# Kernel optimization log

Hardware: AMD Instinct MI355X
Metric: run time of the kernel (lower is better)

Reference implementation:

```python
import jax, jax.numpy as jnp
import numpy as np

N = 50000
F_IN = 256
F_OUT = 256
K = 5
E = 1_600_000
SQRT_2PI = float(np.sqrt(2.0 * np.pi))
SQRT_2 = float(np.sqrt(2.0))


def _ex_relu(mu, sigma):
    # expected value of relu(Normal(mu, sigma)) with sigma = variance
    is_zero = sigma == 0
    safe_sigma = jnp.where(is_zero, 1e-10, sigma)
    sqrt_sigma = jnp.sqrt(safe_sigma)
    w = mu / sqrt_sigma
    nr = sqrt_sigma * (jnp.exp(-0.5 * w * w) / SQRT_2PI
                       + 0.5 * w * (1.0 + jax.lax.erf(w / SQRT_2)))
    return jnp.where(is_zero, jnp.maximum(mu, 0.0), nr)


def _conv(h, src, dst):
    # SimpleConv(aggr='add', combine_root='self_loop'):
    # out[d] = h[d] + sum_{(s,d) in edges} h[s];  h: [K, N, O]
    agg = jnp.zeros_like(h).at[:, dst, :].add(h[:, src, :])
    return h + agg


def setup_inputs() -> dict:
    key = jax.random.key(0)
    ks = jax.random.split(key, 7)
    x = jax.random.normal(ks[0], (N, F_IN), dtype=jnp.float32)
    edges = jax.random.randint(ks[1], (2, E), 0, N, dtype=jnp.int64)
    mask = jax.random.randint(ks[2], (N, F_IN), 0, 2) == 1  # True = missing
    logp = jax.random.normal(ks[3], (K,), dtype=jnp.float32)
    means = jax.random.normal(ks[4], (K, F_IN), dtype=jnp.float32)
    logvars = jax.random.normal(ks[5], (K, F_IN), dtype=jnp.float32)
    weight = jax.random.normal(ks[6], (F_IN, F_OUT), dtype=jnp.float32) * (1.414 / np.sqrt(F_IN + F_OUT) * np.sqrt(6.0))
    bias = jnp.zeros((F_OUT,), dtype=jnp.float32)
    return {"x": x, "edges": edges, "mask": mask, "logp": logp,
            "means": means, "logvars": logvars, "weight": weight, "bias": bias}


def reference(x, edges, mask, logp, means, logvars, weight, bias):
    src, dst = edges[0], edges[1]
    variances = jnp.exp(logvars)                                   # [K, F]
    m = mask[None, :, :]                                           # [1, N, F]
    mean_mat = jnp.where(m, means[:, None, :], x[None, :, :])      # [K, N, F]
    var_mat = jnp.where(m, variances[:, None, :], 0.0)             # [K, N, F]

    transform_x = jnp.einsum('knf,fo->kno', mean_mat, weight) + bias
    transform_covs = jnp.einsum('knf,fo->kno', var_mat, weight * weight)

    conv_x = _conv(transform_x, src, dst)                          # [K, N, O]
    conv_covs = _conv(transform_covs, src, dst)                    # [K, N, O]

    expected_x = _ex_relu(conv_x, conv_covs)                       # [K, N, O]

    # GMM responsibilities over components
    diff2 = (mean_mat - means[:, None, :]) ** 2 / variances[:, None, :]
    log_n = (-0.5 * jnp.sum(diff2, axis=2)
             - 0.5 * F_IN * np.log(2.0 * np.pi)
             - 0.5 * jnp.sum(logvars))                             # [K, N]
    gamma = jax.nn.softmax(logp[:, None] + log_n, axis=0)          # [K, N]

    return jnp.sum(expected_x * gamma[:, :, None], axis=0)         # [N, O]
```

## Files before the change

kernel.cpp:

```cpp
#include <hip/hip_runtime.h>
#include <math.h>

#define F 256
#define KMIX 5
#define RECB 640
#define GR 16
#define GS 3136

typedef __attribute__((ext_vector_type(8))) short bf16x8;
typedef __attribute__((ext_vector_type(4))) float f32x4;

__device__ __forceinline__ float bf2f(unsigned short u) {
  union { unsigned int i; float f; } v; v.i = ((unsigned int)u) << 16; return v.f;
}
__device__ __forceinline__ unsigned short f2bf(float f) {
  union { float f; unsigned int i; } v; v.f = f;
  unsigned int u = v.i;
  unsigned int r = (u + 0x7fffu + ((u >> 16) & 1u)) >> 16;
  return (unsigned short)r;
}

__device__ __forceinline__ f32x4 MFMA(bf16x8 a, bf16x8 b, f32x4 c) {
  return __builtin_amdgcn_mfma_f32_16x16x32_bf16(a, b, c, 0, 0, 0);
}

__device__ __forceinline__ float ex_relu_fast(float mu, float sig) {
  const float c1 = 1.2732395447f;
  const float c2 = 2.5464790895f;
  float t = mu * mu;
  float u = t + c1 * sig;
  float v = t + c2 * sig + 1e-20f;
  float r = __builtin_amdgcn_rsqf(v);
  return 0.5f * mu + 0.5f * u * r;
}

__global__ void kzero(unsigned int* p, long long n) {
  long long i = (long long)blockIdx.x * blockDim.x + threadIdx.x;
  long long stride = (long long)gridDim.x * blockDim.x;
  for (; i < n; i += stride) p[i] = 0u;
}

__global__ __launch_bounds__(256) void k_tab(const float* __restrict__ logvars,
                                             float* __restrict__ ivar) {
  int i = blockIdx.x * 256 + threadIdx.x;
  if (i < KMIX * F) ivar[i] = __expf(-logvars[i]);
}

__global__ __launch_bounds__(256) void k_prep(
    const float* __restrict__ x, const int* __restrict__ mask,
    const float* __restrict__ logp, const float* __restrict__ means,
    const float* __restrict__ ivar,
    unsigned char* __restrict__ rec, float* __restrict__ gamma, int Npad, int N) {
  int wave = threadIdx.x >> 6, lane = threadIdx.x & 63;
  int n = blockIdx.x * 4 + wave;
  if (n >= N) return;
  int f0 = lane * 4;
  const float4 xv4 = *(const float4*)(x + (size_t)n * F + f0);
  const int4 mv4 = *(const int4*)(mask + (size_t)n * F + f0);
  float xv[4] = {xv4.x, xv4.y, xv4.z, xv4.w};
  int mv[4] = {mv4.x, mv4.y, mv4.z, mv4.w};
  unsigned char* rn = rec + (size_t)n * RECB;
  ushort4 xm;
  xm.x = mv[0] ? (unsigned short)0 : f2bf(xv[0]);
  xm.y = mv[1] ? (unsigned short)0 : f2bf(xv[1]);
  xm.z = mv[2] ? (unsigned short)0 : f2bf(xv[2]);
  xm.w = mv[3] ? (unsigned short)0 : f2bf(xv[3]);
  *(ushort4*)(rn + lane * 8) = xm;
  unsigned int nib = (mv[0] ? 1u : 0u) | (mv[1] ? 2u : 0u) |
                     (mv[2] ? 4u : 0u) | (mv[3] ? 8u : 0u);
  unsigned int wbits = nib << ((lane & 7) * 4);
  wbits |= __shfl_xor(wbits, 1, 64);
  wbits |= __shfl_xor(wbits, 2, 64);
  wbits |= __shfl_xor(wbits, 4, 64);
  if ((lane & 7) == 0) *(unsigned int*)(rn + 512 + ((lane >> 3) << 2)) = wbits;
  float lg[KMIX];
#pragma unroll
  for (int k = 0; k < KMIX; ++k) {
    const float4 mk = *(const float4*)(means + k * F + f0);
    const float4 iv = *(const float4*)(ivar + k * F + f0);
    float c = 0.0f, d;
    d = xv[0] - mk.x; c += mv[0] ? 0.0f : d * d * iv.x;
    d = xv[1] - mk.y; c += mv[1] ? 0.0f : d * d * iv.y;
    d = xv[2] - mk.z; c += mv[2] ? 0.0f : d * d * iv.z;
    d = xv[3] - mk.w; c += mv[3] ? 0.0f : d * d * iv.w;
    for (int off = 32; off > 0; off >>= 1) c += __shfl_down(c, off, 64);
    lg[k] = c;
  }
  if (lane == 0) {
    float mx = -1e30f;
#pragma unroll
    for (int k = 0; k < KMIX; ++k) {
      lg[k] = logp[k] - 0.5f * lg[k];
      mx = fmaxf(mx, lg[k]);
    }
    float den = 0.0f, e[KMIX];
#pragma unroll
    for (int k = 0; k < KMIX; ++k) { e[k] = __expf(lg[k] - mx); den += e[k]; }
    float inv = 1.0f / den;
#pragma unroll
    for (int k = 0; k < KMIX; ++k) gamma[k * Npad + n] = e[k] * inv;
  }
}

__global__ void k_count(const int* __restrict__ edges, int* __restrict__ cnt, int E) {
  int i = blockIdx.x * blockDim.x + threadIdx.x;
  if (i < E) {
    int dst = edges[E + i];
    int g = edges[i] / GS;
    atomicAdd(&cnt[dst * GR + g], 1);
  }
}

__global__ __launch_bounds__(1024) void k_scanA(const int* __restrict__ cnt,
                                                int* __restrict__ excl,
                                                int* __restrict__ bsum, int n) {
  __shared__ int s[1024];
  int t = threadIdx.x;
  int i = blockIdx.x * 1024 + t;
  int v = (i < n) ? cnt[i] : 0;
  s[t] = v;
  __syncthreads();
  for (int off = 1; off < 1024; off <<= 1) {
    int u = (t >= off) ? s[t - off] : 0;
    __syncthreads();
    s[t] += u;
    __syncthreads();
  }
  if (i < n) excl[i] = s[t] - v;
  if (t == 1023) bsum[blockIdx.x] = s[1023];
}

__global__ __launch_bounds__(1024) void k_scanB(int* __restrict__ bsum, int nb) {
  __shared__ int s[1024];
  int t = threadIdx.x;
  int v = (t < nb) ? bsum[t] : 0;
  s[t] = v;
  __syncthreads();
  for (int off = 1; off < 1024; off <<= 1) {
    int u = (t >= off) ? s[t - off] : 0;
    __syncthreads();
    s[t] += u;
    __syncthreads();
  }
  if (t < nb) bsum[t] = s[t] - v;
}

__global__ __launch_bounds__(1024) void k_scanC(int* __restrict__ offs,
                                                int* __restrict__ cur,
                                                const int* __restrict__ bsum,
                                                int n, int E) {
  int i = blockIdx.x * 1024 + threadIdx.x;
  if (i < n) {
    int v = offs[i] + bsum[blockIdx.x];
    offs[i] = v;
    cur[i] = v;
  }
  if (i == 0) offs[n] = E;
}

__global__ void k_fill(const int* __restrict__ edges, int* __restrict__ cur,
                       int* __restrict__ srclist, int E) {
  int i = blockIdx.x * blockDim.x + threadIdx.x;
  if (i < E) {
    int src = edges[i];
    int dst = edges[E + i];
    int g = src / GS;
    int pos = atomicAdd(&cur[dst * GR + g], 1);
    srclist[pos] = src;
  }
}

__global__ __launch_bounds__(1024) void k_gather(
    const unsigned char* __restrict__ rec,
    const int* __restrict__ offs, const int* __restrict__ srclist,
    unsigned short* __restrict__ xs_pack, unsigned short* __restrict__ sm_pack,
    float* __restrict__ degp1) {
  __shared__ float xs_l[16][257];
  __shared__ float sm_l[16][257];
  int tile = blockIdx.x;
  int wave = threadIdx.x >> 6, lane = threadIdx.x & 63;
  int fb = lane * 4;
  int n = tile * 16 + wave;
  const unsigned char* rn = rec + (size_t)n * RECB;
  ushort4 xv = *(const ushort4*)(rn + lane * 8);
  unsigned int mw = *(const unsigned int*)(rn + 512 + ((lane >> 3) << 2));
  unsigned int nib = (mw >> ((lane & 7) * 4)) & 0xFu;
  unsigned int macc = (nib | (nib << 7) | (nib << 14) | (nib << 21)) & 0x01010101u;
  float a0 = bf2f(xv.x), a1 = bf2f(xv.y), a2 = bf2f(xv.z), a3 = bf2f(xv.w);
  int s0 = offs[n * GR], s1 = offs[n * GR + GR];
  int i = s0;
  int nsa = 0, nsb = 0, nsc = 0, nsd = 0;
  if (i + 4 <= s1) {
    nsa = srclist[i]; nsb = srclist[i + 1]; nsc = srclist[i + 2]; nsd = srclist[i + 3];
  }
  while (i + 4 <= s1) {
    int sa = nsa, sb = nsb, sc = nsc, sd = nsd;
    const unsigned char* ra = rec + (size_t)sa * RECB;
    const unsigned char* rb = rec + (size_t)sb * RECB;
    const unsigned char* rc = rec + (size_t)sc * RECB;
    const unsigned char* rd = rec + (size_t)sd * RECB;
    ushort4 va = *(const ushort4*)(ra + lane * 8);
    ushort4 vb = *(const ushort4*)(rb + lane * 8);
    ushort4 vc = *(const ushort4*)(rc + lane * 8);
    ushort4 vd = *(const ushort4*)(rd + lane * 8);
    unsigned int wa = *(const unsigned int*)(ra + 512 + ((lane >> 3) << 2));
    unsigned int wb = *(const unsigned int*)(rb + 512 + ((lane >> 3) << 2));
    unsigned int wc = *(const unsigned int*)(rc + 512 + ((lane >> 3) << 2));
    unsigned int wd = *(const unsigned int*)(rd + 512 + ((lane >> 3) << 2));
    i += 4;
    if (i + 4 <= s1) {
      nsa = srclist[i]; nsb = srclist[i + 1]; nsc = srclist[i + 2]; nsd = srclist[i + 3];
    }
    a0 += bf2f(va.x) + bf2f(vb.x) + bf2f(vc.x) + bf2f(vd.x);
    a1 += bf2f(va.y) + bf2f(vb.y) + bf2f(vc.y) + bf2f(vd.y);
    a2 += bf2f(va.z) + bf2f(vb.z) + bf2f(vc.z) + bf2f(vd.z);
    a3 += bf2f(va.w) + bf2f(vb.w) + bf2f(vc.w) + bf2f(vd.w);
    unsigned int na = (wa >> ((lane & 7) * 4)) & 0xFu;
    unsigned int nb = (wb >> ((lane & 7) * 4)) & 0xFu;
    unsigned int nc = (wc >> ((lane & 7) * 4)) & 0xFu;
    unsigned int nd = (wd >> ((lane & 7) * 4)) & 0xFu;
    macc += (na | (na << 7) | (na << 14) | (na << 21)) & 0x01010101u;
    macc += (nb | (nb << 7) | (nb << 14) | (nb << 21)) & 0x01010101u;
    macc += (nc | (nc << 7) | (nc << 14) | (nc << 21)) & 0x01010101u;
    macc += (nd | (nd << 7) | (nd << 14) | (nd << 21)) & 0x01010101u;
  }
  for (; i < s1; ++i) {
    int s = srclist[i];
    const unsigned char* rs = rec + (size_t)s * RECB;
    ushort4 sv = *(const ushort4*)(rs + lane * 8);
    unsigned int ws = *(const unsigned int*)(rs + 512 + ((lane >> 3) << 2));
    a0 += bf2f(sv.x); a1 += bf2f(sv.y); a2 += bf2f(sv.z); a3 += bf2f(sv.w);
    unsigned int ns = (ws >> ((lane & 7) * 4)) & 0xFu;
    macc += (ns | (ns << 7) | (ns << 14) | (ns << 21)) & 0x01010101u;
  }
  xs_l[wave][fb] = a0; xs_l[wave][fb + 1] = a1; xs_l[wave][fb + 2] = a2; xs_l[wave][fb + 3] = a3;
  sm_l[wave][fb] = (float)(macc & 0xFFu);
  sm_l[wave][fb + 1] = (float)((macc >> 8) & 0xFFu);
  sm_l[wave][fb + 2] = (float)((macc >> 16) & 0xFFu);
  sm_l[wave][fb + 3] = (float)(macc >> 24);
  if (lane == 0) degp1[n] = (float)(s1 - s0 + 1);
  __syncthreads();
  if (threadIdx.x < 512) {
    int slot = threadIdx.x;
    int kt = slot >> 6, l = slot & 63;
    int r = l & 15, q = l >> 4;
    int fbase = kt * 32 + q * 8;
    bf16x8 vx, vs;
#pragma unroll
    for (int j = 0; j < 8; ++j) {
      vx[j] = (short)f2bf(xs_l[r][fbase + j]);
      vs[j] = (short)f2bf(sm_l[r][fbase + j]);
    }
    long long po = ((long long)tile * 8 + kt) * 64 + l;
    ((bf16x8*)xs_pack)[po] = vx;
    ((bf16x8*)sm_pack)[po] = vs;
  }
}

__global__ __launch_bounds__(64) void k_bpack(
    const float* __restrict__ weight, const float* __restrict__ means,
    const float* __restrict__ logvars, unsigned short* __restrict__ bpack) {
  int bid = blockIdx.x;
  int kt = bid & 7, ot = (bid >> 3) & 15, m = bid >> 7;
  int l = threadIdx.x;
  int r = l & 15, q = l >> 4;
  int o = ot * 16 + r;
  bf16x8 v;
#pragma unroll
  for (int j = 0; j < 8; ++j) {
    int f = kt * 32 + q * 8 + j;
    float wv = weight[f * F + o];
    float val;
    if (m == 0) val = wv;
    else if (m <= 5) val = means[(m - 1) * F + f] * wv;
    else val = __expf(logvars[(m - 6) * F + f]) * wv * wv;
    v[j] = (short)f2bf(val);
  }
  size_t idx;
  if (m == 0) {
    idx = ((size_t)ot * 8 + kt) * 64 + l;
  } else {
    int s = (m <= 5) ? 0 : 1;
    int k = (m <= 5) ? (m - 1) : (m - 6);
    idx = 8192 + ((((size_t)k * 16 + ot) * 8 + kt) * 64 + l) * 2 + s;
  }
  ((bf16x8*)bpack)[idx] = v;
}

__global__ __launch_bounds__(256, 3) void k_gemm(
    const unsigned short* __restrict__ xs_pack, const unsigned short* __restrict__ sm_pack,
    const unsigned short* __restrict__ bpack, const float* __restrict__ degp1,
    const float* __restrict__ gamma, const float* __restrict__ bias,
    float* __restrict__ out, int N, int Npad, int RB) {
  int L = blockIdx.x;
  int rb = (L >> 5) * 8 + (L & 7);
  int bo = (L >> 3) & 3;
  if (rb >= RB) return;
  __shared__ unsigned char sp_lds[32768];
  int tid = threadIdx.x;
  int wave = tid >> 6, lane = tid & 63;
  int rw = wave >> 1, cw = wave & 1;
  int q = lane >> 4, r16 = lane & 15;
  int rt0 = rb * 4 + rw * 2;
  int ct0 = bo * 4 + cw * 2;
  const bf16x8* XP = (const bf16x8*)xs_pack;
  const bf16x8* BP = (const bf16x8*)bpack;
  const bf16x8* BPp = BP + 8192;

  {
    const uint4* src = (const uint4*)((const unsigned char*)sm_pack + (size_t)rb * 32768) + tid;
    uint4* dst = (uint4*)(void*)sp_lds + tid;
#pragma unroll
    for (int it = 0; it < 8; ++it) dst[it * 256] = src[it * 256];
  }

  f32x4 C1[2][2];
#pragma unroll
  for (int rt = 0; rt < 2; ++rt)
#pragma unroll
    for (int cc = 0; cc < 2; ++cc) C1[rt][cc] = (f32x4){0.f, 0.f, 0.f, 0.f};
#pragma unroll
  for (int kt = 0; kt < 8; ++kt) {
    bf16x8 a0 = XP[((size_t)rt0 * 8 + kt) * 64 + lane];
    bf16x8 a1 = XP[((size_t)(rt0 + 1) * 8 + kt) * 64 + lane];
#pragma unroll
    for (int cc = 0; cc < 2; ++cc) {
      bf16x8 b = BP[((size_t)(ct0 + cc) * 8 + kt) * 64 + lane];
      C1[0][cc] = MFMA(a0, b, C1[0][cc]);
      C1[1][cc] = MFMA(a1, b, C1[1][cc]);
    }
  }

  int row0 = rb * 64 + rw * 32 + q * 4;
  {
    float dp[2][4];
#pragma unroll
    for (int rt = 0; rt < 2; ++rt)
#pragma unroll
      for (int rr = 0; rr < 4; ++rr) dp[rt][rr] = degp1[row0 + rt * 16 + rr];
    float bs[2];
#pragma unroll
    for (int cc = 0; cc < 2; ++cc) bs[cc] = bias[bo * 64 + cw * 32 + cc * 16 + r16];
#pragma unroll
    for (int rt = 0; rt < 2; ++rt)
#pragma unroll
      for (int cc = 0; cc < 2; ++cc)
#pragma unroll
        for (int rr = 0; rr < 4; ++rr) C1[rt][cc][rr] += dp[rt][rr] * bs[cc];
  }

  f32x4 outa[2][2];
#pragma unroll
  for (int rt = 0; rt < 2; ++rt)
#pragma unroll
    for (int cc = 0; cc < 2; ++cc) outa[rt][cc] = (f32x4){0.f, 0.f, 0.f, 0.f};

  __syncthreads();
  const unsigned char* myl = sp_lds + rw * 16384;

  for (int k = 0; k < KMIX; ++k) {
    float gm[2][4];
#pragma unroll
    for (int rt = 0; rt < 2; ++rt)
#pragma unroll
      for (int rr = 0; rr < 4; ++rr) gm[rt][rr] = gamma[k * Npad + row0 + rt * 16 + rr];
    f32x4 ax[2][2], ac[2][2];
#pragma unroll
    for (int rt = 0; rt < 2; ++rt)
#pragma unroll
      for (int cc = 0; cc < 2; ++cc) {
        ax[rt][cc] = C1[rt][cc];
        ac[rt][cc] = (f32x4){0.f, 0.f, 0.f, 0.f};
      }
#pragma unroll
    for (int kt = 0; kt < 8; ++kt) {
      bf16x8 sp0 = *(const bf16x8*)(myl + kt * 1024 + lane * 16);
      bf16x8 sp1 = *(const bf16x8*)(myl + 8192 + kt * 1024 + lane * 16);
#pragma unroll
      for (int cc = 0; cc < 2; ++cc) {
        int c = ct0 + cc;
        const bf16x8* pp = &BPp[((((size_t)k * 16 + c) * 8 + kt) * 64 + lane) * 2];
        bf16x8 bw = pp[0];
        bf16x8 bv = pp[1];
        ax[0][cc] = MFMA(sp0, bw, ax[0][cc]);
        ax[1][cc] = MFMA(sp1, bw, ax[1][cc]);
        ac[0][cc] = MFMA(sp0, bv, ac[0][cc]);
        ac[1][cc] = MFMA(sp1, bv, ac[1][cc]);
      }
    }
#pragma unroll
    for (int rt = 0; rt < 2; ++rt)
#pragma unroll
      for (int cc = 0; cc < 2; ++cc)
#pragma unroll
        for (int rr = 0; rr < 4; ++rr) {
          float e = ex_relu_fast(ax[rt][cc][rr], ac[rt][cc][rr]);
          outa[rt][cc][rr] += gm[rt][rr] * e;
        }
  }

#pragma unroll
  for (int rt = 0; rt < 2; ++rt)
#pragma unroll
    for (int cc = 0; cc < 2; ++cc) {
      int col = bo * 64 + cw * 32 + cc * 16 + r16;
#pragma unroll
      for (int rr = 0; rr < 4; ++rr) {
        int row = row0 + rt * 16 + rr;
        if (row < N) out[(long long)row * F + col] = outa[rt][cc][rr];
      }
    }
}

extern "C" void kernel_launch(void* const* d_in, const int* in_sizes, int n_in,
                              void* d_out, int out_size, void* d_ws, size_t ws_size,
                              hipStream_t stream) {
  const float* x = (const float*)d_in[0];
  const int* edges = (const int*)d_in[1];
  const int* mask = (const int*)d_in[2];
  const float* logp = (const float*)d_in[3];
  const float* means = (const float*)d_in[4];
  const float* logvars = (const float*)d_in[5];
  const float* weight = (const float*)d_in[6];
  const float* bias = (const float*)d_in[7];
  float* out = (float*)d_out;

  int N = in_sizes[0] / F;
  int E = in_sizes[1] / 2;
  int Npad = ((N + 127) / 128) * 128;
  int RB = Npad / 64;
  int NB = N * GR;
  int SB = (NB + 1023) / 1024;

  char* w = (char*)d_ws;
  auto alloc = [&](size_t bytes) {
    char* p = w;
    w += (bytes + 255) & ~(size_t)255;
    return p;
  };
  unsigned char* rec = (unsigned char*)alloc((size_t)N * RECB);
  unsigned short* xsp = (unsigned short*)alloc((size_t)Npad * F * 2);
  unsigned short* smp = (unsigned short*)alloc((size_t)Npad * F * 2);
  unsigned short* bpk = (unsigned short*)alloc((size_t)11 * F * F * 2);
  int* cnt = (int*)alloc((size_t)NB * 4);
  int* offs = (int*)alloc((size_t)(NB + 1) * 4);
  int* cur = (int*)alloc((size_t)NB * 4);
  int* bsum = (int*)alloc((size_t)1024 * 4);
  int* srclist = (int*)alloc((size_t)E * 4);
  float* degp1 = (float*)alloc((size_t)Npad * 4);
  float* gamma = (float*)alloc((size_t)KMIX * Npad * 4);
  float* ivar = (float*)alloc((size_t)KMIX * F * 4);

  kzero<<<782, 256, 0, stream>>>((unsigned int*)cnt, NB);
  k_tab<<<(KMIX * F + 255) / 256, 256, 0, stream>>>(logvars, ivar);
  k_prep<<<(N + 3) / 4, 256, 0, stream>>>(x, mask, logp, means, ivar, rec, gamma, Npad, N);
  k_count<<<(E + 255) / 256, 256, 0, stream>>>(edges, cnt, E);
  k_scanA<<<SB, 1024, 0, stream>>>(cnt, offs, bsum, NB);
  k_scanB<<<1, 1024, 0, stream>>>(bsum, SB);
  k_scanC<<<SB, 1024, 0, stream>>>(offs, cur, bsum, NB, E);
  k_fill<<<(E + 255) / 256, 256, 0, stream>>>(edges, cur, srclist, E);
  k_gather<<<N / 16, 1024, 0, stream>>>(rec, offs, srclist, xsp, smp, degp1);
  k_bpack<<<11 * 16 * 8, 64, 0, stream>>>(weight, means, logvars, bpk);
  int NGG = (RB + 7) / 8;
  k_gemm<<<NGG * 32, 256, 0, stream>>>(xsp, smp, bpk, degp1, gamma, bias, out, N, Npad, RB);
}
```

Before: 682.1 us.

## Fuse setup kernels, merge scan phases, split gather edges across two waves

Merges the zero-fill, inverse-variance table and weight-packing kernels into one launch, and folds the single-block bsum scan into the scan-apply kernel by having every block rescan the block sums. Gather now uses two waves per node, each summing half of the node's edge list. The partial sums are combined through shared memory, which doubles the gather grid and raises memory-level parallelism. This cuts launch count and shortens gather latency per node, at the cost of redundant scan work in each block and extra shared-memory combining.

```diff
diff --git a/kernel.cpp b/kernel.cpp
--- a/kernel.cpp
+++ b/kernel.cpp
@@ -34,16 +34,48 @@
   return 0.5f * mu + 0.5f * u * r;
 }
 
-__global__ void kzero(unsigned int* p, long long n) {
-  long long i = (long long)blockIdx.x * blockDim.x + threadIdx.x;
-  long long stride = (long long)gridDim.x * blockDim.x;
-  for (; i < n; i += stride) p[i] = 0u;
-}
-
-__global__ __launch_bounds__(256) void k_tab(const float* __restrict__ logvars,
-                                             float* __restrict__ ivar) {
-  int i = blockIdx.x * 256 + threadIdx.x;
-  if (i < KMIX * F) ivar[i] = __expf(-logvars[i]);
+__global__ __launch_bounds__(256) void k_setup(
+    const float* __restrict__ logvars, float* __restrict__ ivar,
+    unsigned int* __restrict__ cnt, int NB,
+    const float* __restrict__ weight, const float* __restrict__ means,
+    unsigned short* __restrict__ bpack) {
+  int b = blockIdx.x, tid = threadIdx.x;
+  if (b < 782) {
+#pragma unroll
+    for (int j = 0; j < 4; ++j) {
+      int i = b * 1024 + j * 256 + tid;
+      if (i < NB) cnt[i] = 0u;
+    }
+  } else if (b < 787) {
+    int i = (b - 782) * 256 + tid;
+    if (i < KMIX * F) ivar[i] = __expf(-logvars[i]);
+  } else {
+    int bid = (b - 787) * 4 + (tid >> 6);
+    int l = tid & 63;
+    int kt = bid & 7, ot = (bid >> 3) & 15, m = bid >> 7;
+    int r = l & 15, q = l >> 4;
+    int o = ot * 16 + r;
+    bf16x8 v;
+#pragma unroll
+    for (int j = 0; j < 8; ++j) {
+      int f = kt * 32 + q * 8 + j;
+      float wv = weight[f * F + o];
+      float val;
+      if (m == 0) val = wv;
+      else if (m <= 5) val = means[(m - 1) * F + f] * wv;
+      else val = __expf(logvars[(m - 6) * F + f]) * wv * wv;
+      v[j] = (short)f2bf(val);
+    }
+    size_t idx;
+    if (m == 0) {
+      idx = ((size_t)ot * 8 + kt) * 64 + l;
+    } else {
+      int s = (m <= 5) ? 0 : 1;
+      int k = (m <= 5) ? (m - 1) : (m - 6);
+      idx = 8192 + ((((size_t)k * 16 + ot) * 8 + kt) * 64 + l) * 2 + s;
+    }
+    ((bf16x8*)bpack)[idx] = v;
+  }
 }
 
 __global__ __launch_bounds__(256) void k_prep(
@@ -130,7 +162,10 @@
   if (t == 1023) bsum[blockIdx.x] = s[1023];
 }
 
-__global__ __launch_bounds__(1024) void k_scanB(int* __restrict__ bsum, int nb) {
+__global__ __launch_bounds__(1024) void k_scanC2(int* __restrict__ offs,
+                                                 int* __restrict__ cur,
+                                                 const int* __restrict__ bsum,
+                                                 int n, int E, int nb) {
   __shared__ int s[1024];
   int t = threadIdx.x;
   int v = (t < nb) ? bsum[t] : 0;
@@ -142,18 +177,12 @@
     s[t] += u;
     __syncthreads();
   }
-  if (t < nb) bsum[t] = s[t] - v;
-}
-
-__global__ __launch_bounds__(1024) void k_scanC(int* __restrict__ offs,
-                                                int* __restrict__ cur,
-                                                const int* __restrict__ bsum,
-                                                int n, int E) {
-  int i = blockIdx.x * 1024 + threadIdx.x;
+  int prefix = (blockIdx.x == 0) ? 0 : s[blockIdx.x - 1];
+  int i = blockIdx.x * 1024 + t;
   if (i < n) {
-    int v = offs[i] + bsum[blockIdx.x];
-    offs[i] = v;
-    cur[i] = v;
+    int v2 = offs[i] + prefix;
+    offs[i] = v2;
+    cur[i] = v2;
   }
   if (i == 0) offs[n] = E;
 }
@@ -175,25 +204,34 @@
     const int* __restrict__ offs, const int* __restrict__ srclist,
     unsigned short* __restrict__ xs_pack, unsigned short* __restrict__ sm_pack,
     float* __restrict__ degp1) {
-  __shared__ float xs_l[16][257];
-  __shared__ float sm_l[16][257];
-  int tile = blockIdx.x;
+  __shared__ float xs_l[8][2][257];
+  __shared__ float sm_l[8][2][257];
+  int b = blockIdx.x;
+  int tile = b >> 1, p = b & 1;
   int wave = threadIdx.x >> 6, lane = threadIdx.x & 63;
+  int ln = wave >> 1, h = wave & 1;
+  int n = tile * 16 + p * 8 + ln;
   int fb = lane * 4;
-  int n = tile * 16 + wave;
-  const unsigned char* rn = rec + (size_t)n * RECB;
-  ushort4 xv = *(const ushort4*)(rn + lane * 8);
-  unsigned int mw = *(const unsigned int*)(rn + 512 + ((lane >> 3) << 2));
-  unsigned int nib = (mw >> ((lane & 7) * 4)) & 0xFu;
-  unsigned int macc = (nib | (nib << 7) | (nib << 14) | (nib << 21)) & 0x01010101u;
-  float a0 = bf2f(xv.x), a1 = bf2f(xv.y), a2 = bf2f(xv.z), a3 = bf2f(xv.w);
+  float a0 = 0.f, a1 = 0.f, a2 = 0.f, a3 = 0.f;
+  unsigned int macc = 0u;
   int s0 = offs[n * GR], s1 = offs[n * GR + GR];
-  int i = s0;
+  int len = s1 - s0, mid = s0 + (len >> 1);
+  int i = h ? mid : s0;
+  int e = h ? s1 : mid;
+  if (h == 0) {
+    const unsigned char* rn = rec + (size_t)n * RECB;
+    ushort4 xv = *(const ushort4*)(rn + lane * 8);
+    unsigned int mw = *(const unsigned int*)(rn + 512 + ((lane >> 3) << 2));
+    unsigned int nib = (mw >> ((lane & 7) * 4)) & 0xFu;
+    macc = (nib | (nib << 7) | (nib << 14) | (nib << 21)) & 0x01010101u;
+    a0 = bf2f(xv.x); a1 = bf2f(xv.y); a2 = bf2f(xv.z); a3 = bf2f(xv.w);
+    if (lane == 0) degp1[n] = (float)(len + 1);
+  }
   int nsa = 0, nsb = 0, nsc = 0, nsd = 0;
-  if (i + 4 <= s1) {
+  if (i + 4 <= e) {
     nsa = srclist[i]; nsb = srclist[i + 1]; nsc = srclist[i + 2]; nsd = srclist[i + 3];
   }
-  while (i + 4 <= s1) {
+  while (i + 4 <= e) {
     int sa = nsa, sb = nsb, sc = nsc, sd = nsd;
     const unsigned char* ra = rec + (size_t)sa * RECB;
     const unsigned char* rb = rec + (size_t)sb * RECB;
@@ -208,7 +246,7 @@
     unsigned int wc = *(const unsigned int*)(rc + 512 + ((lane >> 3) << 2));
     unsigned int wd = *(const unsigned int*)(rd + 512 + ((lane >> 3) << 2));
     i += 4;
-    if (i + 4 <= s1) {
+    if (i + 4 <= e) {
       nsa = srclist[i]; nsb = srclist[i + 1]; nsc = srclist[i + 2]; nsd = srclist[i + 3];
     }
     a0 += bf2f(va.x) + bf2f(vb.x) + bf2f(vc.x) + bf2f(vd.x);
@@ -224,7 +262,7 @@
     macc += (nc | (nc << 7) | (nc << 14) | (nc << 21)) & 0x01010101u;
     macc += (nd | (nd << 7) | (nd << 14) | (nd << 21)) & 0x01010101u;
   }
-  for (; i < s1; ++i) {
+  for (; i < e; ++i) {
     int s = srclist[i];
     const unsigned char* rs = rec + (size_t)s * RECB;
     ushort4 sv = *(const ushort4*)(rs + lane * 8);
@@ -233,58 +271,31 @@
     unsigned int ns = (ws >> ((lane & 7) * 4)) & 0xFu;
     macc += (ns | (ns << 7) | (ns << 14) | (ns << 21)) & 0x01010101u;
   }
-  xs_l[wave][fb] = a0; xs_l[wave][fb + 1] = a1; xs_l[wave][fb + 2] = a2; xs_l[wave][fb + 3] = a3;
-  sm_l[wave][fb] = (float)(macc & 0xFFu);
-  sm_l[wave][fb + 1] = (float)((macc >> 8) & 0xFFu);
-  sm_l[wave][fb + 2] = (float)((macc >> 16) & 0xFFu);
-  sm_l[wave][fb + 3] = (float)(macc >> 24);
-  if (lane == 0) degp1[n] = (float)(s1 - s0 + 1);
+  xs_l[ln][h][fb] = a0; xs_l[ln][h][fb + 1] = a1;
+  xs_l[ln][h][fb + 2] = a2; xs_l[ln][h][fb + 3] = a3;
+  sm_l[ln][h][fb] = (float)(macc & 0xFFu);
+  sm_l[ln][h][fb + 1] = (float)((macc >> 8) & 0xFFu);
+  sm_l[ln][h][fb + 2] = (float)((macc >> 16) & 0xFFu);
+  sm_l[ln][h][fb + 3] = (float)(macc >> 24);
   __syncthreads();
   if (threadIdx.x < 512) {
     int slot = threadIdx.x;
     int kt = slot >> 6, l = slot & 63;
     int r = l & 15, q = l >> 4;
-    int fbase = kt * 32 + q * 8;
-    bf16x8 vx, vs;
-#pragma unroll
-    for (int j = 0; j < 8; ++j) {
-      vx[j] = (short)f2bf(xs_l[r][fbase + j]);
-      vs[j] = (short)f2bf(sm_l[r][fbase + j]);
-    }
-    long long po = ((long long)tile * 8 + kt) * 64 + l;
-    ((bf16x8*)xs_pack)[po] = vx;
-    ((bf16x8*)sm_pack)[po] = vs;
-  }
-}
-
-__global__ __launch_bounds__(64) void k_bpack(
-    const float* __restrict__ weight, const float* __restrict__ means,
-    const float* __restrict__ logvars, unsigned short* __restrict__ bpack) {
-  int bid = blockIdx.x;
-  int kt = bid & 7, ot = (bid >> 3) & 15, m = bid >> 7;
-  int l = threadIdx.x;
-  int r = l & 15, q = l >> 4;
-  int o = ot * 16 + r;
-  bf16x8 v;
-#pragma unroll
-  for (int j = 0; j < 8; ++j) {
-    int f = kt * 32 + q * 8 + j;
-    float wv = weight[f * F + o];
-    float val;
-    if (m == 0) val = wv;
-    else if (m <= 5) val = means[(m - 1) * F + f] * wv;
-    else val = __expf(logvars[(m - 6) * F + f]) * wv * wv;
-    v[j] = (short)f2bf(val);
-  }
-  size_t idx;
-  if (m == 0) {
-    idx = ((size_t)ot * 8 + kt) * 64 + l;
-  } else {
-    int s = (m <= 5) ? 0 : 1;
-    int k = (m <= 5) ? (m - 1) : (m - 6);
-    idx = 8192 + ((((size_t)k * 16 + ot) * 8 + kt) * 64 + l) * 2 + s;
-  }
-  ((bf16x8*)bpack)[idx] = v;
+    if ((r >> 3) == p) {
+      int lnn = r & 7;
+      int fbase = kt * 32 + q * 8;
+      bf16x8 vx, vs;
+#pragma unroll
+      for (int j = 0; j < 8; ++j) {
+        vx[j] = (short)f2bf(xs_l[lnn][0][fbase + j] + xs_l[lnn][1][fbase + j]);
+        vs[j] = (short)f2bf(sm_l[lnn][0][fbase + j] + sm_l[lnn][1][fbase + j]);
+      }
+      long long po = ((long long)tile * 8 + kt) * 64 + l;
+      ((bf16x8*)xs_pack)[po] = vx;
+      ((bf16x8*)sm_pack)[po] = vs;
+    }
+  }
 }
 
 __global__ __launch_bounds__(256, 3) void k_gemm(
@@ -451,16 +462,14 @@
   float* gamma = (float*)alloc((size_t)KMIX * Npad * 4);
   float* ivar = (float*)alloc((size_t)KMIX * F * 4);
 
-  kzero<<<782, 256, 0, stream>>>((unsigned int*)cnt, NB);
-  k_tab<<<(KMIX * F + 255) / 256, 256, 0, stream>>>(logvars, ivar);
+  k_setup<<<787 + 352, 256, 0, stream>>>(logvars, ivar, (unsigned int*)cnt, NB,
+                                         weight, means, bpk);
   k_prep<<<(N + 3) / 4, 256, 0, stream>>>(x, mask, logp, means, ivar, rec, gamma, Npad, N);
   k_count<<<(E + 255) / 256, 256, 0, stream>>>(edges, cnt, E);
   k_scanA<<<SB, 1024, 0, stream>>>(cnt, offs, bsum, NB);
-  k_scanB<<<1, 1024, 0, stream>>>(bsum, SB);
-  k_scanC<<<SB, 1024, 0, stream>>>(offs, cur, bsum, NB, E);
+  k_scanC2<<<SB, 1024, 0, stream>>>(offs, cur, bsum, NB, E, SB);
   k_fill<<<(E + 255) / 256, 256, 0, stream>>>(edges, cur, srclist, E);
-  k_gather<<<N / 16, 1024, 0, stream>>>(rec, offs, srclist, xsp, smp, degp1);
-  k_bpack<<<11 * 16 * 8, 64, 0, stream>>>(weight, means, logvars, bpk);
+  k_gather<<<(N / 16) * 2, 1024, 0, stream>>>(rec, offs, srclist, xsp, smp, degp1);
   int NGG = (RB + 7) / 8;
   k_gemm<<<NGG * 32, 256, 0, stream>>>(xsp, smp, bpk, degp1, gamma, bias, out, N, Npad, RB);
 }
```

After: 686.3 us. About the same (+0.6%).
